# Performance work log

Hardware: AMD Instinct MI355X
Metric: run time of the kernel (lower is better)

Reference implementation:

```python
import jax, jax.numpy as jnp
import numpy as np

EMBED = 1024
HEADS = 16
HEAD_DIM = EMBED // HEADS
B, S = 2, 2048


def setup_inputs() -> dict:
    key = jax.random.key(0)
    ks = jax.random.split(key, 11)
    sc = 1.0 / np.sqrt(EMBED)
    d = {
        'query': jax.random.normal(ks[0], (B, S, EMBED), jnp.float32),
        'key':   jax.random.normal(ks[1], (B, S, EMBED), jnp.float32),
        'value': jax.random.normal(ks[2], (B, S, EMBED), jnp.float32),
        'Wq': jax.random.normal(ks[3], (EMBED, EMBED), jnp.float32) * sc,
        'bq': jnp.zeros((EMBED,), jnp.float32),
        'Wk': jax.random.normal(ks[4], (EMBED, EMBED), jnp.float32) * sc,
        'bk': jnp.zeros((EMBED,), jnp.float32),
        'Wv': jax.random.normal(ks[5], (EMBED, EMBED), jnp.float32) * sc,
        'bv': jnp.zeros((EMBED,), jnp.float32),
        'Wo': jax.random.normal(ks[6], (EMBED, EMBED), jnp.float32) * sc,
        'bo': jnp.zeros((EMBED,), jnp.float32),
    }
    return d


def _split_heads(x):
    b, s, _ = x.shape
    return x.reshape(b, s, HEADS, HEAD_DIM).transpose(0, 2, 1, 3)  # [B,H,S,D]


def reference(query, key, value, Wq, bq, Wk, bk, Wv, bv, Wo, bo):
    # nn.Linear: y = x @ W^T + b
    q = _split_heads(query @ Wq.T + bq)
    k = _split_heads(key @ Wk.T + bk)
    v = _split_heads(value @ Wv.T + bv)
    scale = 1.0 / np.sqrt(HEAD_DIM).astype(np.float32)
    attn = jnp.einsum('bhqd,bhkd->bhqk', q, k) * scale  # [B,H,S,S]
    attn = jax.nn.softmax(attn, axis=-1)
    out = jnp.einsum('bhqk,bhkd->bhqd', attn, v)
    out = out.transpose(0, 2, 1, 3).reshape(query.shape[0], -1, EMBED)
    return out @ Wo.T + bo
```

## Files before the change

kernel.cpp:

```cpp
#include <hip/hip_runtime.h>

typedef _Float16 f16;
typedef __fp16   fp16n2 __attribute__((ext_vector_type(2)));
typedef _Float16 f16x8 __attribute__((ext_vector_type(8)));
typedef float    f32x2 __attribute__((ext_vector_type(2)));
typedef float    f32x4 __attribute__((ext_vector_type(4)));
typedef float    f32x16 __attribute__((ext_vector_type(16)));
typedef int      i32x2 __attribute__((ext_vector_type(2)));
typedef unsigned short u16;
typedef unsigned long long u64;

#define B_ 2
#define S_ 2048
#define E_ 1024
#define H_ 16
#define D_ 64
#define M_ (B_*S_)
#define LOG2E 1.44269504088896340736f

__device__ __forceinline__ f32x4 mfma16(f16x8 a, f16x8 b, f32x4 c) {
  return __builtin_amdgcn_mfma_f32_16x16x32_f16(a, b, c, 0, 0, 0);
}
__device__ __forceinline__ f32x16 mfma32(f16x8 a, f16x8 b, f32x16 c) {
  return __builtin_amdgcn_mfma_f32_32x32x16_f16(a, b, c, 0, 0, 0);
}

__device__ __forceinline__ void gload_lds16(const void* g, void* l) {
  __builtin_amdgcn_global_load_lds(
      (const __attribute__((address_space(1))) unsigned int*)g,
      (__attribute__((address_space(3))) unsigned int*)l, 16, 0, 0);
}

__device__ __forceinline__ int pkrtz(float a, float b) {
  union { fp16n2 h; int i; } u;
  u.h = __builtin_amdgcn_cvt_pkrtz(a, b);
  return u.i;
}

__device__ __forceinline__ u16 f16bits(float x) {
  union { f16 h; u16 u; } c; c.h = (f16)x; return c.u;
}

__device__ __forceinline__ f32x16 Z16() {
  f32x16 z = {0.f,0.f,0.f,0.f,0.f,0.f,0.f,0.f,0.f,0.f,0.f,0.f,0.f,0.f,0.f,0.f};
  return z;
}

__device__ __forceinline__ f32x2 pr2(const f32x16& v, int j) {
  return (f32x2){v[2 * j], v[2 * j + 1]};
}

__global__ __launch_bounds__(256) void cast_all(
    const float* __restrict__ q, const float* __restrict__ k, const float* __restrict__ v,
    const float* __restrict__ wq, const float* __restrict__ wk,
    const float* __restrict__ wv, const float* __restrict__ wo,
    f16* __restrict__ xq, f16* __restrict__ xk, f16* __restrict__ xv,
    f16* __restrict__ wqh, f16* __restrict__ wkh, f16* __restrict__ wvh,
    f16* __restrict__ woh) {
  int i = blockIdx.x * 256 + threadIdx.x;
  const float* src; f16* dst; int off;
  if (i < 3 * 524288) {
    int seg = i >> 19; off = i & 524287;
    src = seg == 0 ? q : seg == 1 ? k : v;
    dst = seg == 0 ? xq : seg == 1 ? xk : xv;
  } else {
    int j = i - 3 * 524288;
    int seg = j >> 17; off = j & 131071;
    src = seg == 0 ? wq : seg == 1 ? wk : seg == 2 ? wv : wo;
    dst = seg == 0 ? wqh : seg == 1 ? wkh : seg == 2 ? wvh : woh;
  }
  const float4* s = (const float4*)src;
  float4 a = s[off * 2], b = s[off * 2 + 1];
  f16x8 o = { (f16)a.x, (f16)a.y, (f16)a.z, (f16)a.w,
              (f16)b.x, (f16)b.y, (f16)b.z, (f16)b.w };
  *(f16x8*)&dst[(size_t)off * 8] = o;
}

__device__ __forceinline__ void gemm_core(const f16* __restrict__ A,
                                          const f16* __restrict__ Bm,
                                          f32x4 (&acc)[4][4]) {
  __shared__ f16 Al[128 * 32];
  __shared__ f16 Bl[128 * 32];
  const int tid = threadIdx.x;
  const int w = tid >> 6, lane = tid & 63, lg = lane >> 4, ll = lane & 15;
  const int m0 = blockIdx.x * 128, n0 = blockIdx.y * 128;
  const int wr = (w >> 1) * 64, wc = (w & 1) * 64;

  const f32x4 zero4 = {0.f, 0.f, 0.f, 0.f};
#pragma unroll
  for (int m = 0; m < 4; ++m)
#pragma unroll
    for (int n = 0; n < 4; ++n) acc[m][n] = zero4;

  for (int k0 = 0; k0 < 1024; k0 += 32) {
    __syncthreads();
#pragma unroll
    for (int it = 0; it < 2; ++it) {
      int chunk = it * 256 + w * 64 + lane;
      int row = chunk >> 2;
      int c8  = (chunk & 3) * 8;
      gload_lds16(&A [(size_t)(m0 + row) * 1024 + k0 + c8], &Al[(it * 256 + w * 64) * 8]);
      gload_lds16(&Bm[(size_t)(n0 + row) * 1024 + k0 + c8], &Bl[(it * 256 + w * 64) * 8]);
    }
    __syncthreads();

    f16x8 af[4], bf[4];
#pragma unroll
    for (int m = 0; m < 4; ++m) af[m] = *(const f16x8*)&Al[(wr + m * 16 + ll) * 32 + lg * 8];
#pragma unroll
    for (int n = 0; n < 4; ++n) bf[n] = *(const f16x8*)&Bl[(wc + n * 16 + ll) * 32 + lg * 8];
#pragma unroll
    for (int m = 0; m < 4; ++m)
#pragma unroll
      for (int n = 0; n < 4; ++n) acc[m][n] = mfma16(af[m], bf[n], acc[m][n]);
  }
}

__global__ __launch_bounds__(256) void gemm_qkv(
    const f16* __restrict__ Xq, const f16* __restrict__ Xk, const f16* __restrict__ Xv,
    const f16* __restrict__ Wq, const f16* __restrict__ Wk, const f16* __restrict__ Wv,
    const float* __restrict__ bq, const float* __restrict__ bk, const float* __restrict__ bv,
    f16* __restrict__ Qb, f16* __restrict__ Kb, f16* __restrict__ Vt) {
  const int z = blockIdx.z;
  const f16*   A    = (z == 0) ? Xq : (z == 1) ? Xk : Xv;
  const f16*   Bm   = (z == 0) ? Wq : (z == 1) ? Wk : Wv;
  const float* bias = (z == 0) ? bq : (z == 1) ? bk : bv;
  const float scale = (z == 0) ? (0.125f * LOG2E) : 1.0f;

  f32x4 acc[4][4];
  gemm_core(A, Bm, acc);

  const int tid = threadIdx.x;
  const int w = tid >> 6, lane = tid & 63, lg = lane >> 4, ll = lane & 15;
  const int m0 = blockIdx.x * 128, n0 = blockIdx.y * 128;
  const int wr = (w >> 1) * 64, wc = (w & 1) * 64;

  if (z == 2) {
#pragma unroll
    for (int m = 0; m < 4; ++m)
#pragma unroll
      for (int n = 0; n < 4; ++n) {
        int col = n0 + wc + n * 16 + ll;
        float bv_ = bias[col];
        int h = col >> 6, d = col & 63;
        int rowb = m0 + wr + m * 16 + lg * 4;
        int b = rowb >> 11, s = rowb & 2047;
        u64 pk = (u64)f16bits(acc[m][n][0] + bv_)
               | ((u64)f16bits(acc[m][n][1] + bv_) << 16)
               | ((u64)f16bits(acc[m][n][2] + bv_) << 32)
               | ((u64)f16bits(acc[m][n][3] + bv_) << 48);
        *(u64*)&Vt[(((size_t)(b * H_ + h)) * D_ + d) * S_ + s] = pk;
      }
    return;
  }

  f16* dst = (z == 0) ? Qb : Kb;
#pragma unroll
  for (int m = 0; m < 4; ++m)
#pragma unroll
    for (int n = 0; n < 4; ++n) {
      int col = n0 + wc + n * 16 + ll;
      float bv_ = bias[col];
      int h = col >> 6, d = col & 63;
#pragma unroll
      for (int r = 0; r < 4; ++r) {
        int row = m0 + wr + m * 16 + lg * 4 + r;
        int b = row >> 11, s = row & 2047;
        float v = (acc[m][n][r] + bv_) * scale;
        dst[(((size_t)(b * H_ + h)) * S_ + s) * D_ + d] = (f16)v;
      }
    }
}

__global__ __launch_bounds__(256) void gemm_out(const f16* __restrict__ A,
                                                const f16* __restrict__ W,
                                                const float* __restrict__ bias,
                                                float* __restrict__ out) {
  f32x4 acc[4][4];
  gemm_core(A, W, acc);
  const int tid = threadIdx.x;
  const int w = tid >> 6, lane = tid & 63, lg = lane >> 4, ll = lane & 15;
  const int m0 = blockIdx.x * 128, n0 = blockIdx.y * 128;
  const int wr = (w >> 1) * 64, wc = (w & 1) * 64;
#pragma unroll
  for (int m = 0; m < 4; ++m)
#pragma unroll
    for (int n = 0; n < 4; ++n) {
      int col = n0 + wc + n * 16 + ll;
      float bv_ = bias[col];
#pragma unroll
      for (int r = 0; r < 4; ++r) {
        int row = m0 + wr + m * 16 + lg * 4 + r;
        out[(size_t)row * 1024 + col] = acc[m][n][r] + bv_;
      }
    }
}

__global__ __launch_bounds__(512, 4) void attn_fwd(const f16* __restrict__ Q,
                                                   const f16* __restrict__ K,
                                                   const f16* __restrict__ VT,
                                                   f16* __restrict__ O) {
  const int qt = blockIdx.x, bh = blockIdx.y;
  const int tid = threadIdx.x;
  const int w = tid >> 6, lane = tid & 63;
  const int ql = lane & 31, hi = lane >> 5;
  const int qsub = w & 3, kvh = w >> 2;

  __shared__ __align__(16) char smem[65536];
  char* hbase = smem + kvh * 32768;

  const f16* Qb = Q  + (size_t)bh * S_ * D_;
  const f16* Kb = K  + (size_t)bh * S_ * D_ + (size_t)(kvh * 1024) * D_;
  const f16* Vb = VT + (size_t)bh * D_ * S_ + kvh * 1024;
  const int q0 = qt * 128 + qsub * 32;

  f16x8 qf[4];
#pragma unroll
  for (int ks = 0; ks < 4; ++ks)
    qf[ks] = *(const f16x8*)&Qb[(size_t)(q0 + ql) * 64 + ks * 16 + hi * 8];

  f32x16 accO[2];
  accO[0] = Z16(); accO[1] = Z16();
  float m_r = -1e30f, l_r = 0.f;

  const int seg = w & 3;
  const int lr = lane >> 3;
  const int lc = lane & 7;
  const int cs = lc ^ lr;

#define STAGE(kt_)                                                             \
  {                                                                            \
    char* Kl_ = hbase + ((kt_) & 1) * 16384;                                   \
    char* Vl_ = Kl_ + 8192;                                                    \
    _Pragma("unroll")                                                          \
    for (int i_ = 0; i_ < 2; ++i_) {                                           \
      int r_ = seg * 16 + i_ * 8 + lr;                         \
      gload_lds16(&Kb[(size_t)((kt_) * 64 + r_) * 64 + cs * 8],                \
                  Kl_ + seg * 2048 + i_ * 1024);                               \
      gload_lds16(&Vb[(size_t)r_ * S_ + (kt_) * 64 + cs * 8],                  \
                  Vl_ + seg * 2048 + i_ * 1024);                               \
    }                                                                          \
  }

  STAGE(0);

#pragma unroll 1
  for (int kt = 0; kt < 16; ++kt) {
    __syncthreads();
    if (kt + 1 < 16) STAGE(kt + 1);

    char* KlB = hbase + (kt & 1) * 16384;
    char* VlB = KlB + 8192;

    f32x16 accS[2];
    __builtin_amdgcn_s_setprio(1);
#pragma unroll
    for (int c = 0; c < 2; ++c) {
      int row = c * 32 + ql;
      int rb = row * 128, sw = (row & 7) << 4;
      f16x8 kf0 = *(const f16x8*)(KlB + rb + ((hi * 16) ^ sw));
      accS[c] = mfma32(kf0, qf[0], Z16());
#pragma unroll
      for (int ks = 1; ks < 4; ++ks) {
        f16x8 kf = *(const f16x8*)(KlB + rb + (((ks * 2 + hi) * 16) ^ sw));
        accS[c] = mfma32(kf, qf[ks], accS[c]);
      }
    }
    __builtin_amdgcn_s_setprio(0);

    f32x2 mj[8];
#pragma unroll
    for (int j = 0; j < 8; ++j)
      mj[j] = __builtin_elementwise_max(pr2(accS[0], j), pr2(accS[1], j));
#pragma unroll
    for (int j = 0; j < 4; ++j)
      mj[j] = __builtin_elementwise_max(mj[j], mj[j + 4]);
    mj[0] = __builtin_elementwise_max(mj[0], mj[2]);
    mj[1] = __builtin_elementwise_max(mj[1], mj[3]);
    mj[0] = __builtin_elementwise_max(mj[0], mj[1]);
    float t = fmaxf(mj[0].x, mj[0].y);
    t = fmaxf(t, __shfl_xor(t, 32));

    if (__any(t > m_r + 8.0f)) {
      float mnew = fmaxf(m_r, t);
      float alpha = __builtin_amdgcn_exp2f(m_r - mnew);
      l_r *= alpha;
      accO[0] = accO[0] * alpha;
      accO[1] = accO[1] * alpha;
      m_r = mnew;
    }
    const f32x2 mb = {m_r, m_r};
    f32x2 rs2 = {0.f, 0.f};
#pragma unroll
    for (int c = 0; c < 2; ++c)
#pragma unroll
      for (int j = 0; j < 8; ++j) {
        f32x2 xp = pr2(accS[c], j) - mb;
        float p0 = __builtin_amdgcn_exp2f(xp.x);
        float p1 = __builtin_amdgcn_exp2f(xp.y);
        accS[c][2 * j]     = p0;
        accS[c][2 * j + 1] = p1;
        rs2 += (f32x2){p0, p1};
      }
    float rs = rs2.x + rs2.y;
    rs += __shfl_xor(rs, 32);
    l_r += rs;

#pragma unroll
    for (int c = 0; c < 2; ++c)
#pragma unroll
      for (int s = 0; s < 2; ++s) {
        int b0 = s * 8;
        int a0 = pkrtz(accS[c][b0 + 0], accS[c][b0 + 1]);
        int a1 = pkrtz(accS[c][b0 + 2], accS[c][b0 + 3]);
        int a2 = pkrtz(accS[c][b0 + 4], accS[c][b0 + 5]);
        int a3 = pkrtz(accS[c][b0 + 6], accS[c][b0 + 7]);
        i32x2 r02 = __builtin_amdgcn_permlane32_swap(a0, a2, false, false);
        i32x2 r13 = __builtin_amdgcn_permlane32_swap(a1, a3, false, false);
        union { int i[4]; f16x8 h; } pf;
        pf.i[0] = r02.x; pf.i[1] = r13.x; pf.i[2] = r02.y; pf.i[3] = r13.y;
        int kvb = c * 64 + s * 32 + hi * 16;
        __builtin_amdgcn_s_setprio(1);
#pragma unroll
        for (int dc = 0; dc < 2; ++dc) {
          int dr = dc * 32 + ql;
          f16x8 vf = *(const f16x8*)(VlB + dr * 128 + (kvb ^ ((dr & 7) << 4)));
          accO[dc] = mfma32(vf, pf.h, accO[dc]);
        }
        __builtin_amdgcn_s_setprio(0);
      }
  }
#undef STAGE

  __syncthreads();
  float* mlB = (float*)smem;
  if (kvh == 1) {
    if (hi == 0) {
      mlB[qsub * 64 + ql * 2]     = m_r;
      mlB[qsub * 64 + ql * 2 + 1] = l_r;
    }
#pragma unroll
    for (int dc = 0; dc < 2; ++dc)
#pragma unroll
      for (int g = 0; g < 4; ++g) {
        int d0 = g * 8 + hi * 4 + dc * 32;
        f32x4 v = { accO[dc][g * 4 + 0], accO[dc][g * 4 + 1],
                    accO[dc][g * 4 + 2], accO[dc][g * 4 + 3] };
        *(f32x4*)(smem + 32768 + qsub * 8192 + ql * 256 + ((d0 * 4) ^ ((ql & 7) << 4))) = v;
      }
  }
  __syncthreads();
  f16* Ep = (f16*)(smem + 1024);
  if (kvh == 0) {
    float m2 = mlB[qsub * 64 + ql * 2], l2 = mlB[qsub * 64 + ql * 2 + 1];
    float mm = fmaxf(m_r, m2);
    float a1 = __builtin_amdgcn_exp2f(m_r - mm), a2 = __builtin_amdgcn_exp2f(m2 - mm);
    float inv = 1.0f / (l_r * a1 + l2 * a2);
    a1 *= inv; a2 *= inv;
#pragma unroll
    for (int dc = 0; dc < 2; ++dc)
#pragma unroll
      for (int g = 0; g < 4; ++g) {
        int d0 = g * 8 + hi * 4 + dc * 32;
        f32x4 o2 = *(const f32x4*)(smem + 32768 + qsub * 8192 + ql * 256 +
                                   ((d0 * 4) ^ ((ql & 7) << 4)));
        u64 pk = (u64)f16bits(accO[dc][g * 4 + 0] * a1 + o2[0] * a2)
               | ((u64)f16bits(accO[dc][g * 4 + 1] * a1 + o2[1] * a2) << 16)
               | ((u64)f16bits(accO[dc][g * 4 + 2] * a1 + o2[2] * a2) << 32)
               | ((u64)f16bits(accO[dc][g * 4 + 3] * a1 + o2[3] * a2) << 48);
        *(u64*)&Ep[(qsub * 32 + ql) * 68 + d0] = pk;
      }
  }
  __syncthreads();
  const int b = bh >> 4, h = bh & 15;
#pragma unroll
  for (int pass = 0; pass < 2; ++pass) {
    int idx = pass * 512 + tid;
    int row = idx >> 3, cx = idx & 7;
    f16x8 v = *(const f16x8*)&Ep[row * 68 + cx * 8];
    *(f16x8*)&O[((size_t)(b * S_ + qt * 128 + row)) * E_ + h * 64 + cx * 8] = v;
  }
}

extern "C" void kernel_launch(void* const* d_in, const int* in_sizes, int n_in,
                              void* d_out, int out_size, void* d_ws, size_t ws_size,
                              hipStream_t stream) {
  (void)in_sizes; (void)n_in; (void)out_size; (void)ws_size;
  const float* q  = (const float*)d_in[0];
  const float* k  = (const float*)d_in[1];
  const float* v  = (const float*)d_in[2];
  const float* Wq = (const float*)d_in[3];
  const float* bq = (const float*)d_in[4];
  const float* Wk = (const float*)d_in[5];
  const float* bk = (const float*)d_in[6];
  const float* Wv = (const float*)d_in[7];
  const float* bv = (const float*)d_in[8];
  const float* Wo = (const float*)d_in[9];
  const float* bo = (const float*)d_in[10];
  float* out = (float*)d_out;

  f16* ws  = (f16*)d_ws;
  f16* Xq  = ws;
  f16* Xk  = Xq  + (size_t)M_ * E_;
  f16* Xv  = Xk  + (size_t)M_ * E_;
  f16* Wqh = Xv  + (size_t)M_ * E_;
  f16* Wkh = Wqh + (size_t)E_ * E_;
  f16* Wvh = Wkh + (size_t)E_ * E_;
  f16* Woh = Wvh + (size_t)E_ * E_;
  f16* Qb  = Woh + (size_t)E_ * E_;
  f16* Kb  = Qb  + (size_t)M_ * E_;
  f16* VTb = Kb  + (size_t)M_ * E_;
  f16* AO  = Xq;

  cast_all<<<8192, 256, 0, stream>>>(q, k, v, Wq, Wk, Wv, Wo,
                                     Xq, Xk, Xv, Wqh, Wkh, Wvh, Woh);

  gemm_qkv<<<dim3(M_ / 128, E_ / 128, 3), 256, 0, stream>>>(
      Xq, Xk, Xv, Wqh, Wkh, Wvh, bq, bk, bv, Qb, Kb, VTb);

  attn_fwd<<<dim3(S_ / 128, B_ * H_), 512, 0, stream>>>(Qb, Kb, VTb, AO);

  gemm_out<<<dim3(M_ / 128, E_ / 128), 256, 0, stream>>>(AO, Woh, bo, out);
}
```

Baseline: 139.5 us.

## Double-buffer LDS tiles in GEMM core to overlap global loads with MFMA

The shared GEMM core, used by the projection GEMMs, now keeps two LDS buffers for the A and B tiles. The first K-slice is loaded before the loop. Each iteration then issues the asynchronous global-to-LDS load for the next slice and runs MFMAs on the current one, so one barrier per iteration replaces two. This aims to hide global load latency behind compute, at the cost of twice the LDS per block. It also relies on the barrier waiting for outstanding vector loads, and the compiler may still insert conservative waits that limit the overlap.

```diff
diff --git a/kernel.cpp b/kernel.cpp
--- a/kernel.cpp
+++ b/kernel.cpp
@@ -79,8 +79,8 @@
 __device__ __forceinline__ void gemm_core(const f16* __restrict__ A,
                                           const f16* __restrict__ Bm,
                                           f32x4 (&acc)[4][4]) {
-  __shared__ f16 Al[128 * 32];
-  __shared__ f16 Bl[128 * 32];
+  __shared__ f16 Al[2][128 * 32];
+  __shared__ f16 Bl[2][128 * 32];
   const int tid = threadIdx.x;
   const int w = tid >> 6, lane = tid & 63, lg = lane >> 4, ll = lane & 15;
   const int m0 = blockIdx.x * 128, n0 = blockIdx.y * 128;
@@ -92,28 +92,39 @@
 #pragma unroll
     for (int n = 0; n < 4; ++n) acc[m][n] = zero4;
 
+#define GSTAGE(k0_)                                                            \
+  {                                                                            \
+    const int bi_ = ((k0_) >> 5) & 1;                                          \
+    _Pragma("unroll")                                                          \
+    for (int it = 0; it < 2; ++it) {                                           \
+      int chunk = it * 256 + w * 64 + lane;                                    \
+      int row = chunk >> 2;                                                    \
+      int c8  = (chunk & 3) * 8;                                               \
+      gload_lds16(&A [(size_t)(m0 + row) * 1024 + (k0_) + c8],                 \
+                  &Al[bi_][(it * 256 + w * 64) * 8]);                          \
+      gload_lds16(&Bm[(size_t)(n0 + row) * 1024 + (k0_) + c8],                 \
+                  &Bl[bi_][(it * 256 + w * 64) * 8]);                          \
+    }                                                                          \
+  }
+
+  GSTAGE(0);
+
   for (int k0 = 0; k0 < 1024; k0 += 32) {
     __syncthreads();
-#pragma unroll
-    for (int it = 0; it < 2; ++it) {
-      int chunk = it * 256 + w * 64 + lane;
-      int row = chunk >> 2;
-      int c8  = (chunk & 3) * 8;
-      gload_lds16(&A [(size_t)(m0 + row) * 1024 + k0 + c8], &Al[(it * 256 + w * 64) * 8]);
-      gload_lds16(&Bm[(size_t)(n0 + row) * 1024 + k0 + c8], &Bl[(it * 256 + w * 64) * 8]);
-    }
-    __syncthreads();
+    if (k0 + 32 < 1024) GSTAGE(k0 + 32);
+    const int bi = (k0 >> 5) & 1;
 
     f16x8 af[4], bf[4];
 #pragma unroll
-    for (int m = 0; m < 4; ++m) af[m] = *(const f16x8*)&Al[(wr + m * 16 + ll) * 32 + lg * 8];
-#pragma unroll
-    for (int n = 0; n < 4; ++n) bf[n] = *(const f16x8*)&Bl[(wc + n * 16 + ll) * 32 + lg * 8];
+    for (int m = 0; m < 4; ++m) af[m] = *(const f16x8*)&Al[bi][(wr + m * 16 + ll) * 32 + lg * 8];
+#pragma unroll
+    for (int n = 0; n < 4; ++n) bf[n] = *(const f16x8*)&Bl[bi][(wc + n * 16 + ll) * 32 + lg * 8];
 #pragma unroll
     for (int m = 0; m < 4; ++m)
 #pragma unroll
       for (int n = 0; n < 4; ++n) acc[m][n] = mfma16(af[m], bf[n], acc[m][n]);
   }
+#undef GSTAGE
 }
 
 __global__ __launch_bounds__(256) void gemm_qkv(
```

Result: slower. 144.2 us (+3.4%).
